# Optimization experiments

Hardware: AMD Instinct MI355X
Metric: run time of the kernel (lower is better)

The kernel has to match this reference:

```python
import jax, jax.numpy as jnp
import numpy as np

S = 512       # opt.resize_shape
DEPTH = 2     # opt.cattn_depth -> pooling window 2**DEPTH
P = 8         # opt.cattn_patch


def _interp_matrix(src, dst):
    # 1-D bilinear interpolation matrix, align_corners=True (matches F.interpolate)
    pos = jnp.linspace(0.0, src - 1.0, dst)
    lo = jnp.floor(pos).astype(jnp.int32)
    hi = jnp.minimum(lo + 1, src - 1)
    w = (pos - lo).astype(jnp.float32)
    idx = jnp.arange(dst)
    M = jnp.zeros((dst, src), jnp.float32)
    M = M.at[idx, lo].add(1.0 - w).at[idx, hi].add(w)
    return M


def setup_inputs() -> dict:
    key = jax.random.key(0)
    k1, k2, k3, k4 = jax.random.split(key, 4)
    x = jax.random.normal(k1, (4, 256, 64, 64), jnp.float32)
    attentions = jax.random.uniform(k2, (4, 8, 4096, 256), jnp.float32)
    conv_w = jax.random.normal(k3, (8, 256), jnp.float32) * 0.05
    conv_b = jax.random.normal(k4, (8,), jnp.float32) * 0.05
    return {"x": x, "attentions": attentions, "conv_w": conv_w, "conv_b": conv_b}


def reference(x, attentions, conv_w, conv_b):
    B, _, H, W = x.shape
    C = conv_w.shape[0]
    Kp = 2 ** DEPTH
    # 1x1 conv (ConvX)
    y = jnp.einsum('bchw,oc->bohw', x, conv_w) + conv_b[None, :, None, None]
    # bilinear upsample to (S, S), align_corners=True, separable matrices
    Mh, Mw = _interp_matrix(H, S), _interp_matrix(W, S)
    y = jnp.einsum('bchw,sh,tw->bcst', y, Mh, Mw)  # [B,C,S,S]
    # argmax one-hot (scatter of ones along class dim)
    am = jnp.argmax(y, axis=1)  # [B,S,S]
    onehot = (am[:, None] == jnp.arange(C)[None, :, None, None]).astype(y.dtype)
    # grouped conv of ones / Kp^2 == Kp x Kp mean pooling
    Sm = S // Kp
    fm = onehot.reshape(B, C, Sm, Kp, Sm, Kp).mean(axis=(3, 5))  # [B,C,Sm,Sm]
    # non-overlapping unfold PxP -> [B,C,P*P,L], torch Unfold ordering
    Lh = Sm // P
    unf = fm.reshape(B, C, Lh, P, Lh, P).transpose(0, 1, 3, 5, 2, 4).reshape(B, C, P * P, Lh * Lh)
    # per-class normalized attention matmul (vectorized over classes)
    nz = jnp.count_nonzero(attentions, axis=-1).astype(y.dtype)[..., None] + 1e-5  # [B,C,Q,1]
    corr = jnp.einsum('bcqk,bcpk->bcqp', attentions / nz, unf)  # [B,C,Q,P*P]
    # fold back to [B,C,S,S] (non-overlapping patches)
    Qh = S // P
    corr = corr.reshape(B, C, Qh, Qh, P, P).transpose(0, 1, 2, 4, 3, 5).reshape(B, C, S, S)
    out = jax.nn.log_softmax((corr + 1.0) * y, axis=1)
    return out, attentions
```

## Files before the change

### kernel.cpp

```cpp
#include <hip/hip_runtime.h>
#include <cstdint>

__global__ __launch_bounds__(256) void k_conv(const float* __restrict__ x,
                                              const float* __restrict__ w,
                                              const float* __restrict__ bias,
                                              float* __restrict__ y) {
  __shared__ float wl[2048];
  __shared__ float red[4][64][9];
  const int tid = threadIdx.x;
#pragma unroll
  for (int i = 0; i < 8; i++) { int idx = tid + i * 256; wl[idx] = w[idx]; }
  const int bi = blockIdx.x >> 6, row = blockIdx.x & 63;
  const int hwi = tid & 63, cg = tid >> 6;
  const float* xp = x + (((size_t)(bi * 256 + cg * 64)) * 64 + row) * 64 + hwi;
  float acc[8] = {0.f, 0.f, 0.f, 0.f, 0.f, 0.f, 0.f, 0.f};
  __syncthreads();
#pragma unroll 4
  for (int c = 0; c < 64; c++) {
    float v = xp[(size_t)c * 4096];
#pragma unroll
    for (int o = 0; o < 8; o++) acc[o] += v * wl[o * 256 + cg * 64 + c];
  }
#pragma unroll
  for (int o = 0; o < 8; o++) red[cg][hwi][o] = acc[o];
  __syncthreads();
#pragma unroll
  for (int i = 0; i < 2; i++) {
    int p = tid + i * 256; int o = p >> 6, hw = p & 63;
    float sv = red[0][hw][o] + red[1][hw][o] + red[2][hw][o] + red[3][hw][o] + bias[o];
    y[(((size_t)(bi * 8 + o)) * 64 + row) * 64 + hw] = sv;
  }
}

__global__ __launch_bounds__(256) void k_pool(const float* __restrict__ ys,
                                              float* __restrict__ fm) {
  const int g = blockIdx.x * 256 + threadIdx.x;
  const int bi = g >> 14, rem = g & 16383;
  const int sm = rem >> 7, tm = rem & 127;
  int cnt[8] = {0, 0, 0, 0, 0, 0, 0, 0};
  const float* yb = ys + (size_t)bi * 8 * 4096;
#pragma unroll
  for (int py = 0; py < 4; py++) {
    const int s = sm * 4 + py;
    float ph = s * (63.0f / 511.0f); int lh = (int)ph; float wh = ph - (float)lh;
    const int dh = (lh < 63) ? 64 : 0;
#pragma unroll
    for (int px = 0; px < 4; px++) {
      const int t = tm * 4 + px;
      float pw = t * (63.0f / 511.0f); int lt = (int)pw; float wt = pw - (float)lt;
      const int dt = (lt < 63) ? 1 : 0;
      const float w00 = (1.f - wh) * (1.f - wt), w01 = (1.f - wh) * wt;
      const float w10 = wh * (1.f - wt), w11 = wh * wt;
      const int base = lh * 64 + lt;
      float best = 0.f; int am = 0;
#pragma unroll
      for (int c = 0; c < 8; c++) {
        const float* yc = yb + c * 4096 + base;
        float v = w00 * yc[0] + w01 * yc[dt] + w10 * yc[dh] + w11 * yc[dh + dt];
        if (c == 0) { best = v; } else if (v > best) { best = v; am = c; }
      }
#pragma unroll
      for (int c = 0; c < 8; c++) cnt[c] += (am == c);
    }
  }
  const size_t ob = ((size_t)bi * 8) << 14;
#pragma unroll
  for (int c = 0; c < 8; c++)
    fm[ob + ((size_t)c << 14) + (sm << 7) + tm] = (float)cnt[c] * (1.0f / 16.0f);
}

__global__ __launch_bounds__(256, 2) void k_corr(const float* __restrict__ A,
                                                 const float* __restrict__ fm,
                                                 float* __restrict__ Aout,
                                                 float* __restrict__ corr,
                                                 float* __restrict__ nzinv) {
  __shared__ __align__(16) float At[32][260];
  __shared__ __align__(16) float Uts[32][64];
  __shared__ int nzc[256];
  const int tid = threadIdx.x;
  const int bc = blockIdx.y;
  const int qb = blockIdx.x << 8;
  const float* Ab = A + ((size_t)bc * 4096 + qb) * 256;
  float* Ob = Aout + ((size_t)bc * 4096 + qb) * 256;
  const float* fmb = fm + ((size_t)bc << 14);
  nzc[tid] = 0;
  const int pg = tid & 7, qg = tid >> 3;
  const int p0 = pg << 3, q0 = qg << 3;

  int fq[8], fk[8], ul[8], up[8];
#pragma unroll
  for (int i = 0; i < 8; i++) {
    const int f = tid + (i << 8);
    fq[i] = f >> 3; fk[i] = (f & 7) << 2;
    ul[i] = f >> 6; up[i] = f & 63;
  }

  float4 ar[8]; float ur[8];
#pragma unroll
  for (int i = 0; i < 8; i++) ar[i] = *(const float4*)(Ab + (size_t)fq[i] * 256 + fk[i]);
#pragma unroll
  for (int i = 0; i < 8; i++) {
    const int l = ul[i], p = up[i];
    ur[i] = fmb[((l >> 4) * 8 + (p >> 3)) * 128 + (l & 15) * 8 + (p & 7)];
  }
  __syncthreads();
#pragma unroll
  for (int i = 0; i < 8; i++) {
    At[fk[i] + 0][fq[i]] = ar[i].x; At[fk[i] + 1][fq[i]] = ar[i].y;
    At[fk[i] + 2][fq[i]] = ar[i].z; At[fk[i] + 3][fq[i]] = ar[i].w;
    *(float4*)(Ob + (size_t)fq[i] * 256 + fk[i]) = ar[i];
    int c4 = (ar[i].x != 0.f) + (ar[i].y != 0.f) + (ar[i].z != 0.f) + (ar[i].w != 0.f);
    c4 += __shfl_xor(c4, 1); c4 += __shfl_xor(c4, 2); c4 += __shfl_xor(c4, 4);
    if ((tid & 7) == 0) atomicAdd(&nzc[fq[i]], c4);
    Uts[ul[i]][up[i]] = ur[i];
  }
  __syncthreads();

  float acc[8][8];
#pragma unroll
  for (int j = 0; j < 8; j++)
#pragma unroll
    for (int i = 0; i < 8; i++) acc[j][i] = 0.f;

  for (int c = 0; c < 8; c++) {
    if (c < 7) {
      const int kc = (c + 1) << 5;
#pragma unroll
      for (int i = 0; i < 8; i++) ar[i] = *(const float4*)(Ab + (size_t)fq[i] * 256 + kc + fk[i]);
#pragma unroll
      for (int i = 0; i < 8; i++) {
        const int l = kc + ul[i], p = up[i];
        ur[i] = fmb[((l >> 4) * 8 + (p >> 3)) * 128 + (l & 15) * 8 + (p & 7)];
      }
    }
#pragma unroll 8
    for (int kk = 0; kk < 32; kk++) {
      float4 a0 = *(const float4*)&At[kk][q0];
      float4 a1 = *(const float4*)&At[kk][q0 + 4];
      float4 u0 = *(const float4*)&Uts[kk][p0];
      float4 u1 = *(const float4*)&Uts[kk][p0 + 4];
      const float av[8] = {a0.x, a0.y, a0.z, a0.w, a1.x, a1.y, a1.z, a1.w};
      const float uv[8] = {u0.x, u0.y, u0.z, u0.w, u1.x, u1.y, u1.z, u1.w};
#pragma unroll
      for (int j = 0; j < 8; j++)
#pragma unroll
        for (int i = 0; i < 8; i++) acc[j][i] += av[j] * uv[i];
    }
    __syncthreads();
    if (c < 7) {
      const int kc = (c + 1) << 5;
#pragma unroll
      for (int i = 0; i < 8; i++) {
        At[fk[i] + 0][fq[i]] = ar[i].x; At[fk[i] + 1][fq[i]] = ar[i].y;
        At[fk[i] + 2][fq[i]] = ar[i].z; At[fk[i] + 3][fq[i]] = ar[i].w;
        *(float4*)(Ob + (size_t)fq[i] * 256 + kc + fk[i]) = ar[i];
        int c4 = (ar[i].x != 0.f) + (ar[i].y != 0.f) + (ar[i].z != 0.f) + (ar[i].w != 0.f);
        c4 += __shfl_xor(c4, 1); c4 += __shfl_xor(c4, 2); c4 += __shfl_xor(c4, 4);
        if ((tid & 7) == 0) atomicAdd(&nzc[fq[i]], c4);
        Uts[ul[i]][up[i]] = ur[i];
      }
    }
    __syncthreads();
  }

  nzinv[(size_t)bc * 4096 + qb + tid] = 1.0f / ((float)nzc[tid] + 1e-5f);

#pragma unroll
  for (int j = 0; j < 8; j++) {
    float* cb = corr + (((size_t)bc * 4096 + qb + q0 + j) << 6) + p0;
    *(float4*)cb       = make_float4(acc[j][0], acc[j][1], acc[j][2], acc[j][3]);
    *(float4*)(cb + 4) = make_float4(acc[j][4], acc[j][5], acc[j][6], acc[j][7]);
  }
}

__global__ __launch_bounds__(256) void k_out(const float* __restrict__ corr,
                                             const float* __restrict__ nzinv,
                                             const float* __restrict__ ys,
                                             float* __restrict__ out) {
  __shared__ float G[2][8][65];
  const int bx = blockIdx.x;
  const int b = bx >> 8;
  const int s0 = (bx & 255) << 1;
  const int tid = threadIdx.x;
  const float* ysb = ys + ((size_t)b << 15);
#pragma unroll
  for (int j = 0; j < 4; j++) {
    const int e = tid + (j << 8);
    const int sl = e >> 9, c = (e >> 6) & 7, l = e & 63;
    const int s = s0 + sl;
    float ph = s * (63.0f / 511.0f); int lh = (int)ph; float wh = ph - (float)lh;
    const int dh = (lh < 63) ? 64 : 0;
    const float* yc = ysb + ((size_t)c << 12) + lh * 64 + l;
    G[sl][c][l] = (1.f - wh) * yc[0] + wh * yc[dh];
  }
  __syncthreads();

  const int sl = tid >> 7;
  const int s = s0 + sl;
  const int t0 = (tid & 127) << 2;
  const int q = ((s >> 3) << 6) + (t0 >> 3);
  const int p0 = ((s & 7) << 3) + (t0 & 7);

  float z[4][8];
#pragma unroll
  for (int c = 0; c < 8; c++) {
    const size_t bcp = (size_t)(b * 8 + c);
    const float4 cr = *(const float4*)&corr[(((bcp << 12) + q) << 6) + p0];
    const float rz = nzinv[(bcp << 12) + q];
    const float crv[4] = {cr.x, cr.y, cr.z, cr.w};
#pragma unroll
    for (int u = 0; u < 4; u++) {
      const float pw = (t0 + u) * (63.0f / 511.0f);
      const int lt = (int)pw; const float wtt = pw - (float)lt;
      const int hi = (lt < 63) ? lt + 1 : 63;
      const float yv = (1.f - wtt) * G[sl][c][lt] + wtt * G[sl][c][hi];
      z[u][c] = (crv[u] * rz + 1.0f) * yv;
    }
  }
  const size_t ob = ((size_t)b << 21) + ((size_t)s << 9) + t0;
#pragma unroll
  for (int c = 0; c < 8; c++) {
    float4 o;
#pragma unroll
    for (int u = 0; u < 4; u++) {
      float m = z[u][0];
#pragma unroll
      for (int cc = 1; cc < 8; cc++) m = fmaxf(m, z[u][cc]);
      float sum = 0.f;
#pragma unroll
      for (int cc = 0; cc < 8; cc++) sum += __expf(z[u][cc] - m);
      const float v = z[u][c] - m - __logf(sum);
      if (u == 0) o.x = v; else if (u == 1) o.y = v; else if (u == 2) o.z = v; else o.w = v;
    }
    *(float4*)&out[ob + ((size_t)c << 18)] = o;
  }
}

extern "C" void kernel_launch(void* const* d_in, const int* in_sizes, int n_in,
                              void* d_out, int out_size, void* d_ws, size_t ws_size,
                              hipStream_t stream) {
  const float* x   = (const float*)d_in[0];
  const float* att = (const float*)d_in[1];
  const float* cw  = (const float*)d_in[2];
  const float* cb  = (const float*)d_in[3];
  float* out1 = (float*)d_out;
  float* out2 = out1 + (size_t)4 * 8 * 512 * 512;
  float* ws = (float*)d_ws;
  float* y_small = ws;
  float* fm      = ws + 131072;
  float* nzinv   = ws + 655360;
  float* corr    = ws + 786432;

  k_conv<<<256, 256, 0, stream>>>(x, cw, cb, y_small);
  k_pool<<<256, 256, 0, stream>>>(y_small, fm);
  dim3 g4(16, 32);
  k_corr<<<g4, 256, 0, stream>>>(att, fm, out2, corr, nzinv);
  k_out<<<1024, 256, 0, stream>>>(corr, nzinv, y_small, out1);
}
```

Before: 332.7 us.

## Compute attention-unfold correlation with bf16 MFMA and direct global A loads

Rewrites k_corr to convert the attention rows and the pooled class map to bf16 and run 16x16x32 MFMA instructions instead of FP32 FMA through shared-memory tiles. The unfold matrix is staged once per block in swizzled shared memory, A fragments are read straight from global memory, and the nonzero count per query row is done with a wavefront reduction instead of shared atomics. Blocks now cover 128 queries, which doubles the grid. The change trades FP32 accuracy for bf16 in the matmul, which risks numerical drift, and the kernel stays dominated by the large attention copy and read traffic.

```diff
diff --git a/kernel.cpp b/kernel.cpp
--- a/kernel.cpp
+++ b/kernel.cpp
@@ -1,5 +1,16 @@
 #include <hip/hip_runtime.h>
 #include <cstdint>
+
+typedef __attribute__((ext_vector_type(8))) short short8_t;
+typedef __attribute__((ext_vector_type(4))) float f32x4;
+
+static __device__ __forceinline__ unsigned bf16_rne(float x) {
+  union { float f; unsigned u; } a; a.f = x;
+  return (a.u + 0x7FFFu + ((a.u >> 16) & 1u)) >> 16;
+}
+static __device__ __forceinline__ unsigned pk2(float lo, float hi) {
+  return bf16_rne(lo) | (bf16_rne(hi) << 16);
+}
 
 __global__ __launch_bounds__(256) void k_conv(const float* __restrict__ x,
                                               const float* __restrict__ w,
@@ -69,107 +80,101 @@
     fm[ob + ((size_t)c << 14) + (sm << 7) + tm] = (float)cnt[c] * (1.0f / 16.0f);
 }
 
-__global__ __launch_bounds__(256, 2) void k_corr(const float* __restrict__ A,
-                                                 const float* __restrict__ fm,
-                                                 float* __restrict__ Aout,
-                                                 float* __restrict__ corr,
-                                                 float* __restrict__ nzinv) {
-  __shared__ __align__(16) float At[32][260];
-  __shared__ __align__(16) float Uts[32][64];
-  __shared__ int nzc[256];
+__global__ __launch_bounds__(256) void k_corr(const float* __restrict__ A,
+                                              const float* __restrict__ fm,
+                                              float* __restrict__ Aout,
+                                              float* __restrict__ corr,
+                                              float* __restrict__ nzinv) {
+  __shared__ unsigned short Ubt[64 * 256];
   const int tid = threadIdx.x;
   const int bc = blockIdx.y;
-  const int qb = blockIdx.x << 8;
+  const int qb = blockIdx.x << 7;
   const float* Ab = A + ((size_t)bc * 4096 + qb) * 256;
   float* Ob = Aout + ((size_t)bc * 4096 + qb) * 256;
   const float* fmb = fm + ((size_t)bc << 14);
-  nzc[tid] = 0;
-  const int pg = tid & 7, qg = tid >> 3;
-  const int p0 = pg << 3, q0 = qg << 3;
-
-  int fq[8], fk[8], ul[8], up[8];
-#pragma unroll
-  for (int i = 0; i < 8; i++) {
-    const int f = tid + (i << 8);
-    fq[i] = f >> 3; fk[i] = (f & 7) << 2;
-    ul[i] = f >> 6; up[i] = f & 63;
-  }
-
-  float4 ar[8]; float ur[8];
-#pragma unroll
-  for (int i = 0; i < 8; i++) ar[i] = *(const float4*)(Ab + (size_t)fq[i] * 256 + fk[i]);
-#pragma unroll
-  for (int i = 0; i < 8; i++) {
-    const int l = ul[i], p = up[i];
-    ur[i] = fmb[((l >> 4) * 8 + (p >> 3)) * 128 + (l & 15) * 8 + (p & 7)];
-  }
-  __syncthreads();
-#pragma unroll
-  for (int i = 0; i < 8; i++) {
-    At[fk[i] + 0][fq[i]] = ar[i].x; At[fk[i] + 1][fq[i]] = ar[i].y;
-    At[fk[i] + 2][fq[i]] = ar[i].z; At[fk[i] + 3][fq[i]] = ar[i].w;
-    *(float4*)(Ob + (size_t)fq[i] * 256 + fk[i]) = ar[i];
-    int c4 = (ar[i].x != 0.f) + (ar[i].y != 0.f) + (ar[i].z != 0.f) + (ar[i].w != 0.f);
-    c4 += __shfl_xor(c4, 1); c4 += __shfl_xor(c4, 2); c4 += __shfl_xor(c4, 4);
-    if ((tid & 7) == 0) atomicAdd(&nzc[fq[i]], c4);
-    Uts[ul[i]][up[i]] = ur[i];
-  }
-  __syncthreads();
-
-  float acc[8][8];
-#pragma unroll
-  for (int j = 0; j < 8; j++)
-#pragma unroll
-    for (int i = 0; i < 8; i++) acc[j][i] = 0.f;
-
-  for (int c = 0; c < 8; c++) {
-    if (c < 7) {
-      const int kc = (c + 1) << 5;
-#pragma unroll
-      for (int i = 0; i < 8; i++) ar[i] = *(const float4*)(Ab + (size_t)fq[i] * 256 + kc + fk[i]);
-#pragma unroll
-      for (int i = 0; i < 8; i++) {
-        const int l = kc + ul[i], p = up[i];
-        ur[i] = fmb[((l >> 4) * 8 + (p >> 3)) * 128 + (l & 15) * 8 + (p & 7)];
+
+  {
+    const int p = tid >> 2, k0 = (tid & 3) << 6;
+    const int fmbase = ((k0 >> 4) << 10) + ((p >> 3) << 7) + (p & 7);
+    char* ubase = (char*)Ubt + (p << 9);
+    const int sw = (p & 7) << 4;
+#pragma unroll
+    for (int j = 0; j < 64; j += 2) {
+      const float v0 = fmb[fmbase + ((j >> 4) << 10) + ((j & 15) << 3)];
+      const float v1 = fmb[fmbase + (((j + 1) >> 4) << 10) + (((j + 1) & 15) << 3)];
+      *(unsigned*)(ubase + ((((k0 + j) << 1)) ^ sw)) = pk2(v0, v1);
+    }
+  }
+  __syncthreads();
+
+  const int lane = tid & 63, w = tid >> 6;
+  const int m = lane & 15, g = lane >> 4;
+  const float* arow0 = Ab + ((size_t)((w << 5) + m)) * 256 + (g << 3);
+  const float* arow1 = arow0 + 16 * 256;
+  const char* ub = (const char*)Ubt + ((size_t)m << 9);
+  const int sw = (m & 7) << 4;
+  const float4* Ab4 = (const float4*)Ab;
+  float4* Ob4 = (float4*)Ob;
+
+  f32x4 acc[2][4];
+#pragma unroll
+  for (int qf = 0; qf < 2; qf++)
+#pragma unroll
+    for (int pf = 0; pf < 4; pf++) acc[qf][pf] = (f32x4){0.f, 0.f, 0.f, 0.f};
+
+#pragma unroll 2
+  for (int c = 0; c < 8; ++c) {
+    const int kc = c << 5;
+    float4 cp[4];
+#pragma unroll
+    for (int i = 0; i < 4; i++) cp[i] = Ab4[(c << 10) + (i << 8) + tid];
+    const float4 a00 = *(const float4*)(arow0 + kc);
+    const float4 a01 = *(const float4*)(arow0 + kc + 4);
+    const float4 a10 = *(const float4*)(arow1 + kc);
+    const float4 a11 = *(const float4*)(arow1 + kc + 4);
+    const int ka = ((c << 6) + (g << 4)) ^ sw;
+    short8_t bf0 = *(const short8_t*)(ub + ka);
+    short8_t bf1 = *(const short8_t*)(ub + ka + 8192);
+    short8_t bf2 = *(const short8_t*)(ub + ka + 16384);
+    short8_t bf3 = *(const short8_t*)(ub + ka + 24576);
+    union { unsigned u[4]; short8_t s; } fa0, fa1;
+    fa0.u[0] = pk2(a00.x, a00.y); fa0.u[1] = pk2(a00.z, a00.w);
+    fa0.u[2] = pk2(a01.x, a01.y); fa0.u[3] = pk2(a01.z, a01.w);
+    fa1.u[0] = pk2(a10.x, a10.y); fa1.u[1] = pk2(a10.z, a10.w);
+    fa1.u[2] = pk2(a11.x, a11.y); fa1.u[3] = pk2(a11.z, a11.w);
+    acc[0][0] = __builtin_amdgcn_mfma_f32_16x16x32_bf16(fa0.s, bf0, acc[0][0], 0, 0, 0);
+    acc[1][0] = __builtin_amdgcn_mfma_f32_16x16x32_bf16(fa1.s, bf0, acc[1][0], 0, 0, 0);
+    acc[0][1] = __builtin_amdgcn_mfma_f32_16x16x32_bf16(fa0.s, bf1, acc[0][1], 0, 0, 0);
+    acc[1][1] = __builtin_amdgcn_mfma_f32_16x16x32_bf16(fa1.s, bf1, acc[1][1], 0, 0, 0);
+    acc[0][2] = __builtin_amdgcn_mfma_f32_16x16x32_bf16(fa0.s, bf2, acc[0][2], 0, 0, 0);
+    acc[1][2] = __builtin_amdgcn_mfma_f32_16x16x32_bf16(fa1.s, bf2, acc[1][2], 0, 0, 0);
+    acc[0][3] = __builtin_amdgcn_mfma_f32_16x16x32_bf16(fa0.s, bf3, acc[0][3], 0, 0, 0);
+    acc[1][3] = __builtin_amdgcn_mfma_f32_16x16x32_bf16(fa1.s, bf3, acc[1][3], 0, 0, 0);
+#pragma unroll
+    for (int i = 0; i < 4; i++) {
+      Ob4[(c << 10) + (i << 8) + tid] = cp[i];
+      int c4 = (cp[i].x != 0.f) + (cp[i].y != 0.f) + (cp[i].z != 0.f) + (cp[i].w != 0.f);
+      c4 += __shfl_xor(c4, 1);  c4 += __shfl_xor(c4, 2);  c4 += __shfl_xor(c4, 4);
+      c4 += __shfl_xor(c4, 8);  c4 += __shfl_xor(c4, 16); c4 += __shfl_xor(c4, 32);
+      if (lane == 0) {
+        const int row = (c << 4) + (i << 2) + w;
+        nzinv[(size_t)bc * 4096 + qb + row] = 1.0f / ((float)c4 + 1e-5f);
       }
     }
-#pragma unroll 8
-    for (int kk = 0; kk < 32; kk++) {
-      float4 a0 = *(const float4*)&At[kk][q0];
-      float4 a1 = *(const float4*)&At[kk][q0 + 4];
-      float4 u0 = *(const float4*)&Uts[kk][p0];
-      float4 u1 = *(const float4*)&Uts[kk][p0 + 4];
-      const float av[8] = {a0.x, a0.y, a0.z, a0.w, a1.x, a1.y, a1.z, a1.w};
-      const float uv[8] = {u0.x, u0.y, u0.z, u0.w, u1.x, u1.y, u1.z, u1.w};
-#pragma unroll
-      for (int j = 0; j < 8; j++)
-#pragma unroll
-        for (int i = 0; i < 8; i++) acc[j][i] += av[j] * uv[i];
-    }
-    __syncthreads();
-    if (c < 7) {
-      const int kc = (c + 1) << 5;
-#pragma unroll
-      for (int i = 0; i < 8; i++) {
-        At[fk[i] + 0][fq[i]] = ar[i].x; At[fk[i] + 1][fq[i]] = ar[i].y;
-        At[fk[i] + 2][fq[i]] = ar[i].z; At[fk[i] + 3][fq[i]] = ar[i].w;
-        *(float4*)(Ob + (size_t)fq[i] * 256 + kc + fk[i]) = ar[i];
-        int c4 = (ar[i].x != 0.f) + (ar[i].y != 0.f) + (ar[i].z != 0.f) + (ar[i].w != 0.f);
-        c4 += __shfl_xor(c4, 1); c4 += __shfl_xor(c4, 2); c4 += __shfl_xor(c4, 4);
-        if ((tid & 7) == 0) atomicAdd(&nzc[fq[i]], c4);
-        Uts[ul[i]][up[i]] = ur[i];
-      }
-    }
-    __syncthreads();
-  }
-
-  nzinv[(size_t)bc * 4096 + qb + tid] = 1.0f / ((float)nzc[tid] + 1e-5f);
-
-#pragma unroll
-  for (int j = 0; j < 8; j++) {
-    float* cb = corr + (((size_t)bc * 4096 + qb + q0 + j) << 6) + p0;
-    *(float4*)cb       = make_float4(acc[j][0], acc[j][1], acc[j][2], acc[j][3]);
-    *(float4*)(cb + 4) = make_float4(acc[j][4], acc[j][5], acc[j][6], acc[j][7]);
+  }
+
+  const int qrow = (w << 5);
+#pragma unroll
+  for (int qf = 0; qf < 2; qf++) {
+    const int q0r = qb + qrow + (qf << 4) + (g << 2);
+#pragma unroll
+    for (int r = 0; r < 4; r++) {
+      float* cb = corr + (((size_t)bc * 4096 + q0r + r) << 6) + m;
+      cb[0]  = acc[qf][0][r];
+      cb[16] = acc[qf][1][r];
+      cb[32] = acc[qf][2][r];
+      cb[48] = acc[qf][3][r];
+    }
   }
 }
 
@@ -223,13 +228,13 @@
     float4 o;
 #pragma unroll
     for (int u = 0; u < 4; u++) {
-      float m = z[u][0];
-#pragma unroll
-      for (int cc = 1; cc < 8; cc++) m = fmaxf(m, z[u][cc]);
+      float mx = z[u][0];
+#pragma unroll
+      for (int cc = 1; cc < 8; cc++) mx = fmaxf(mx, z[u][cc]);
       float sum = 0.f;
 #pragma unroll
-      for (int cc = 0; cc < 8; cc++) sum += __expf(z[u][cc] - m);
-      const float v = z[u][c] - m - __logf(sum);
+      for (int cc = 0; cc < 8; cc++) sum += __expf(z[u][cc] - mx);
+      const float v = z[u][c] - mx - __logf(sum);
       if (u == 0) o.x = v; else if (u == 1) o.y = v; else if (u == 2) o.z = v; else o.w = v;
     }
     *(float4*)&out[ob + ((size_t)c << 18)] = o;
@@ -253,7 +258,7 @@
 
   k_conv<<<256, 256, 0, stream>>>(x, cw, cb, y_small);
   k_pool<<<256, 256, 0, stream>>>(y_small, fm);
-  dim3 g4(16, 32);
+  dim3 g4(32, 32);
   k_corr<<<g4, 256, 0, stream>>>(att, fm, out2, corr, nzinv);
   k_out<<<1024, 256, 0, stream>>>(corr, nzinv, y_small, out1);
 }
```

Result: no change. 335.5 us (+0.8%).
